# Kernel optimization log

Hardware: AMD Instinct MI355X
Metric: run time of the kernel (lower is better)

Reference implementation:

```python
import jax, jax.numpy as jnp
import numpy as np

NUM_EXPERTS = 32
TOP_K = 4
HIDDEN = 2048
INTER = 768
N_TOKENS = 2048
NORM_TOPK = True


def setup_inputs() -> dict:
    key = jax.random.key(0)
    k0, k1, k2, k3 = jax.random.split(key, 4)
    hidden_states = jax.random.normal(k0, (N_TOKENS, HIDDEN), dtype=jnp.float32)
    # router gate: Linear(hidden, num_experts), stored as (h, E)
    Wg = jax.random.normal(k1, (HIDDEN, NUM_EXPERTS), dtype=jnp.float32) * 0.02
    # per-expert merged gate_up: (E, h, 2*i); down: (E, i, h)
    Wgu = jax.random.normal(k2, (NUM_EXPERTS, HIDDEN, 2 * INTER), dtype=jnp.float32) * 0.02
    Wd = jax.random.normal(k3, (NUM_EXPERTS, INTER, HIDDEN), dtype=jnp.float32) * 0.02
    return {"hidden_states": hidden_states, "Wg": Wg, "Wgu": Wgu, "Wd": Wd}


def reference(hidden_states, Wg, Wgu, Wd):
    E = Wgu.shape[0]
    # ---- routing ----
    router_logits = hidden_states @ Wg                       # (N, E)
    probs = jax.nn.softmax(router_logits.astype(jnp.float32), axis=-1)
    topk_w, topk_idx = jax.lax.top_k(probs, TOP_K)           # (N, K)
    if NORM_TOPK:
        topk_w = topk_w / jnp.sum(topk_w, axis=-1, keepdims=True)
    topk_w = topk_w.astype(hidden_states.dtype)
    # dense combine weights: (N, E), zero where expert not selected
    combine = jnp.einsum("nke,nk->ne", jax.nn.one_hot(topk_idx, E, dtype=topk_w.dtype), topk_w)
    # ---- experts (dense dispatch, zero-weighted combine == gather/scatter math) ----
    gate_up = jnp.einsum("nh,ehf->nef", hidden_states, Wgu)  # (N, E, 2i)
    gate, up = jnp.split(gate_up, 2, axis=-1)                # (N, E, i) each
    y = jax.nn.silu(gate) * up                               # SiluAndMul
    y = y * combine[:, :, None]                              # apply routing weight before down-proj (linear -> equivalent)
    out = jnp.einsum("nef,efh->nh", y, Wd)                   # (N, h)
    return out
```

## Files before the change

kernel.cpp:

```cpp
#include <hip/hip_runtime.h>
#include <hip/hip_bf16.h>

#define NE 32
#define TOPK 4
#define HID 2048
#define INTER 768
#define NT 2048
#define MAXTILE 64

typedef float f32x4 __attribute__((ext_vector_type(4)));
typedef float f32x2 __attribute__((ext_vector_type(2)));
typedef unsigned int u32x4 __attribute__((ext_vector_type(4)));
typedef unsigned int u32x2 __attribute__((ext_vector_type(2)));
typedef short short8 __attribute__((ext_vector_type(8)));
typedef __bf16 bf16x8 __attribute__((ext_vector_type(8)));

__device__ inline unsigned short f2bf(float f) {
  unsigned u = __builtin_bit_cast(unsigned, f);
  u += 0x7fffu + ((u >> 16) & 1u);
  return (unsigned short)(u >> 16);
}
__device__ inline unsigned pack2(unsigned short a, unsigned short b) {
  return (unsigned)a | ((unsigned)b << 16);
}
__device__ inline f32x4 mfma_bf16(short8 a, short8 b, f32x4 c) {
  return __builtin_amdgcn_mfma_f32_16x16x32_bf16(
      __builtin_bit_cast(bf16x8, a), __builtin_bit_cast(bf16x8, b), c, 0, 0, 0);
}
__device__ inline void gload16(const void* g, void* l) {
  __builtin_amdgcn_global_load_lds(
      (const __attribute__((address_space(1))) void*)g,
      (__attribute__((address_space(3))) void*)l, 16, 0, 0);
}
__device__ inline bool locate(const int* __restrict__ counts, int tile, int& e,
                              int& m0, int& base, int& ne) {
  int tl = tile;
  base = 0;
  for (e = 0; e < NE; ++e) {
    const int c = counts[e];
    const int nt = (c + 255) >> 8;
    if (tl < nt) {
      m0 = tl << 8;
      ne = c;
      return true;
    }
    tl -= nt;
    base += c;
  }
  return false;
}

__global__ __launch_bounds__(64) void k_router(const float* __restrict__ X,
                                               const float* __restrict__ Wg,
                                               int* __restrict__ expert_of,
                                               float* __restrict__ weight_of,
                                               int* __restrict__ counts,
                                               unsigned short* __restrict__ Xb) {
  const int n = blockIdx.x;
  const int lane = threadIdx.x;
  const float* x = X + (size_t)n * HID;
  float acc[NE];
#pragma unroll
  for (int e = 0; e < NE; ++e) acc[e] = 0.f;
  for (int h = lane; h < HID; h += 64) {
    const float xv = x[h];
    const f32x4* wr = (const f32x4*)(Wg + (size_t)h * NE);
#pragma unroll
    for (int q = 0; q < NE / 4; ++q) {
      f32x4 w4 = wr[q];
      acc[q * 4 + 0] += xv * w4[0];
      acc[q * 4 + 1] += xv * w4[1];
      acc[q * 4 + 2] += xv * w4[2];
      acc[q * 4 + 3] += xv * w4[3];
    }
  }
  const f32x4* x4 = (const f32x4*)x;
  u32x2* xb2 = (u32x2*)(Xb + (size_t)n * HID);
#pragma unroll
  for (int it = 0; it < HID / 4 / 64; ++it) {
    const int q = it * 64 + lane;
    f32x4 v = x4[q];
    u32x2 t = {pack2(f2bf(v[0]), f2bf(v[1])), pack2(f2bf(v[2]), f2bf(v[3]))};
    xb2[q] = t;
  }
#pragma unroll
  for (int off = 32; off >= 1; off >>= 1) {
#pragma unroll
    for (int e = 0; e < NE; ++e) acc[e] += __shfl_xor(acc[e], off, 64);
  }
  if (lane == 0) {
    float m = acc[0];
#pragma unroll
    for (int e = 1; e < NE; ++e) m = fmaxf(m, acc[e]);
    unsigned used = 0;
    int idx[TOPK];
    float wv[TOPK];
    float wsum = 0.f;
    for (int k = 0; k < TOPK; ++k) {
      int best = 0;
      float bv = -1e30f;
      for (int e = 0; e < NE; ++e) {
        if (!((used >> e) & 1u) && acc[e] > bv) { bv = acc[e]; best = e; }
      }
      used |= 1u << best;
      float w = expf(bv - m);
      idx[k] = best;
      wv[k] = w;
      wsum += w;
    }
    const float inv = 1.f / wsum;
    for (int k = 0; k < TOPK; ++k) {
      expert_of[n * TOPK + k] = idx[k];
      weight_of[n * TOPK + k] = wv[k] * inv;
      atomicAdd(&counts[idx[k]], 1);
    }
  }
}

__global__ __launch_bounds__(64) void k_scatter(const int* __restrict__ expert_of,
                                                const float* __restrict__ weight_of,
                                                const int* __restrict__ counts,
                                                int* __restrict__ slot_token,
                                                float* __restrict__ slot_w) {
  const int e = blockIdx.x;
  const int lane = threadIdx.x;
  int cnt = 0;
  for (int i = 0; i < NE; ++i) cnt += (i < e) ? counts[i] : 0;
  for (int a0 = 0; a0 < NT * TOPK; a0 += 64) {
    const int a = a0 + lane;
    const bool m = (expert_of[a] == e);
    const unsigned long long bal = __ballot(m);
    if (m) {
      const int pos = cnt + __popcll(bal & ((1ull << lane) - 1ull));
      slot_token[pos] = a >> 2;
      slot_w[pos] = weight_of[a];
    }
    cnt += __popcll(bal);
  }
}

__global__ __launch_bounds__(512) void k_gemm1(const unsigned short* __restrict__ Xb,
                                               const float* __restrict__ Wgu,
                                               const int* __restrict__ slot_token,
                                               const float* __restrict__ slot_w,
                                               const int* __restrict__ counts,
                                               unsigned short* __restrict__ Y) {
  int e, m0, base, ne;
  if (!locate(counts, blockIdx.x, e, m0, base, ne)) return;
  const int n0 = blockIdx.y * 64;
  const int tid = threadIdx.x;
  const int lane = tid & 63, w = tid >> 6;
  const int wm = w >> 1, wn = w & 1;
  const int fr = lane & 15, fo = lane >> 4;
  const int lr = lane >> 3, lk = lane & 7;

  __shared__ __attribute__((aligned(16))) unsigned short As[2][256 * 64];
  __shared__ __attribute__((aligned(16))) unsigned short Bg[2][64 * 64];
  __shared__ __attribute__((aligned(16))) unsigned short Bu[2][64 * 64];

  f32x4 accg[4][2], accu[4][2];
#pragma unroll
  for (int i = 0; i < 4; ++i)
#pragma unroll
    for (int j = 0; j < 2; ++j) {
      f32x4 z = {0.f, 0.f, 0.f, 0.f};
      accg[i][j] = z;
      accu[i][j] = z;
    }

  const unsigned short* asrc[4];
#pragma unroll
  for (int i = 0; i < 4; ++i) {
    const int ra = (w * 4 + i) * 8 + lr;
    const int tok = slot_token[base + min(m0 + ra, ne - 1)];
    asrc[i] = Xb + (size_t)tok * HID + ((lk ^ (ra & 7)) << 3);
  }

  const int np = tid & 31, kg = (tid >> 5) & 7, rg = tid >> 8;
  const float* bsrc = Wgu + (size_t)e * HID * (2 * INTER) +
                      (size_t)(kg * 8) * (2 * INTER) + rg * INTER + n0 + 2 * np;
  const int n_a = 2 * np, n_b = 2 * np + 1;
  const int wofa = n_a * 64 + ((kg ^ (n_a & 7)) << 3);
  const int wofb = n_b * 64 + ((kg ^ (n_b & 7)) << 3);

  auto stage_a = [&](int t, int b) {
#pragma unroll
    for (int i = 0; i < 4; ++i) gload16(asrc[i] + t * 64, &As[b][(w * 4 + i) * 512]);
  };
  auto load_b = [&](int t, f32x2* bv) {
    const float* bp = bsrc + (size_t)(t * 64) * (2 * INTER);
#pragma unroll
    for (int j = 0; j < 8; ++j) bv[j] = *(const f32x2*)(bp + (size_t)j * (2 * INTER));
  };
  auto pack_write = [&](const f32x2* bv, int b) {
    u32x4 ta = {pack2(f2bf(bv[0][0]), f2bf(bv[1][0])), pack2(f2bf(bv[2][0]), f2bf(bv[3][0])),
                pack2(f2bf(bv[4][0]), f2bf(bv[5][0])), pack2(f2bf(bv[6][0]), f2bf(bv[7][0]))};
    u32x4 tb = {pack2(f2bf(bv[0][1]), f2bf(bv[1][1])), pack2(f2bf(bv[2][1]), f2bf(bv[3][1])),
                pack2(f2bf(bv[4][1]), f2bf(bv[5][1])), pack2(f2bf(bv[6][1]), f2bf(bv[7][1]))};
    unsigned short* Bd = rg ? Bu[b] : Bg[b];
    *(u32x4*)&Bd[wofa] = ta;
    *(u32x4*)&Bd[wofb] = tb;
  };
  auto do_mfma = [&](int b) {
#pragma unroll
    for (int ks = 0; ks < 2; ++ks) {
      const int c = ks * 4 + fo;
      short8 a[4], bg[2], bu[2];
#pragma unroll
      for (int mi = 0; mi < 4; ++mi) {
        const int row = wm * 64 + mi * 16 + fr;
        a[mi] = *(const short8*)&As[b][row * 64 + ((c ^ (row & 7)) << 3)];
      }
#pragma unroll
      for (int ni = 0; ni < 2; ++ni) {
        const int row = wn * 32 + ni * 16 + fr;
        const int off = row * 64 + ((c ^ (row & 7)) << 3);
        bg[ni] = *(const short8*)&Bg[b][off];
        bu[ni] = *(const short8*)&Bu[b][off];
      }
#pragma unroll
      for (int mi = 0; mi < 4; ++mi)
#pragma unroll
        for (int ni = 0; ni < 2; ++ni) {
          accg[mi][ni] = mfma_bf16(a[mi], bg[ni], accg[mi][ni]);
          accu[mi][ni] = mfma_bf16(a[mi], bu[ni], accu[mi][ni]);
        }
    }
  };

  const int NS = HID / 64;
  {
    f32x2 bv[8];
    stage_a(0, 0);
    load_b(0, bv);
    pack_write(bv, 0);
  }
  __syncthreads();
#pragma unroll 2
  for (int t = 0; t < NS; ++t) {
    const int cur = t & 1, nxt = cur ^ 1;
    f32x2 bv[8];
    const bool more = (t + 1 < NS);
    if (more) {
      stage_a(t + 1, nxt);
      load_b(t + 1, bv);
    }
    __builtin_amdgcn_sched_barrier(0);
    do_mfma(cur);
    if (more) pack_write(bv, nxt);
    __syncthreads();
  }

#pragma unroll
  for (int mi = 0; mi < 4; ++mi) {
#pragma unroll
    for (int j = 0; j < 4; ++j) {
      const int gm = m0 + wm * 64 + mi * 16 + fo * 4 + j;
      if (gm < ne) {
        const float wgt = slot_w[base + gm];
        unsigned short* yp = Y + (size_t)(base + gm) * INTER + n0 + wn * 32;
#pragma unroll
        for (int ni = 0; ni < 2; ++ni) {
          const float g = accg[mi][ni][j];
          const float u = accu[mi][ni][j];
          const float yv = (g / (1.0f + __expf(-g))) * u * wgt;
          yp[ni * 16 + fr] = f2bf(yv);
        }
      }
    }
  }
}

__global__ __launch_bounds__(512) void k_gemm2(const unsigned short* __restrict__ Y,
                                               const float* __restrict__ Wd,
                                               const int* __restrict__ slot_token,
                                               const int* __restrict__ counts,
                                               float* __restrict__ out) {
  int e, m0, base, ne;
  if (!locate(counts, blockIdx.x, e, m0, base, ne)) return;
  const int n0 = blockIdx.y * 128;
  const int tid = threadIdx.x;
  const int lane = tid & 63, w = tid >> 6;
  const int wm = w >> 1, wn = w & 1;
  const int fr = lane & 15, fo = lane >> 4;
  const int lr = lane >> 3, lk = lane & 7;

  __shared__ __attribute__((aligned(16))) unsigned short As[2][256 * 64];
  __shared__ __attribute__((aligned(16))) unsigned short Bs[2][128 * 64];

  f32x4 acc[4][4];
#pragma unroll
  for (int i = 0; i < 4; ++i)
#pragma unroll
    for (int j = 0; j < 4; ++j) {
      f32x4 z = {0.f, 0.f, 0.f, 0.f};
      acc[i][j] = z;
    }

  const unsigned short* asrc[4];
#pragma unroll
  for (int i = 0; i < 4; ++i) {
    const int ra = (w * 4 + i) * 8 + lr;
    const int grow = base + min(m0 + ra, ne - 1);
    asrc[i] = Y + (size_t)grow * INTER + ((lk ^ (ra & 7)) << 3);
  }

  const int np = tid & 63, kg = tid >> 6;
  const float* bsrc = Wd + (size_t)e * INTER * HID + (size_t)(kg * 8) * HID + n0 + 2 * np;
  const int n_a = 2 * np, n_b = 2 * np + 1;
  const int wofa = n_a * 64 + ((kg ^ (n_a & 7)) << 3);
  const int wofb = n_b * 64 + ((kg ^ (n_b & 7)) << 3);

  auto stage_a = [&](int t, int b) {
#pragma unroll
    for (int i = 0; i < 4; ++i) gload16(asrc[i] + t * 64, &As[b][(w * 4 + i) * 512]);
  };
  auto load_b = [&](int t, f32x2* bv) {
    const float* bp = bsrc + (size_t)(t * 64) * HID;
#pragma unroll
    for (int j = 0; j < 8; ++j) bv[j] = *(const f32x2*)(bp + (size_t)j * HID);
  };
  auto pack_write = [&](const f32x2* bv, int b) {
    u32x4 ta = {pack2(f2bf(bv[0][0]), f2bf(bv[1][0])), pack2(f2bf(bv[2][0]), f2bf(bv[3][0])),
                pack2(f2bf(bv[4][0]), f2bf(bv[5][0])), pack2(f2bf(bv[6][0]), f2bf(bv[7][0]))};
    u32x4 tb = {pack2(f2bf(bv[0][1]), f2bf(bv[1][1])), pack2(f2bf(bv[2][1]), f2bf(bv[3][1])),
                pack2(f2bf(bv[4][1]), f2bf(bv[5][1])), pack2(f2bf(bv[6][1]), f2bf(bv[7][1]))};
    *(u32x4*)&Bs[b][wofa] = ta;
    *(u32x4*)&Bs[b][wofb] = tb;
  };
  auto do_mfma = [&](int b) {
#pragma unroll
    for (int ks = 0; ks < 2; ++ks) {
      const int c = ks * 4 + fo;
      short8 a[4], bb[4];
#pragma unroll
      for (int mi = 0; mi < 4; ++mi) {
        const int row = wm * 64 + mi * 16 + fr;
        a[mi] = *(const short8*)&As[b][row * 64 + ((c ^ (row & 7)) << 3)];
      }
#pragma unroll
      for (int ni = 0; ni < 4; ++ni) {
        const int row = wn * 64 + ni * 16 + fr;
        bb[ni] = *(const short8*)&Bs[b][row * 64 + ((c ^ (row & 7)) << 3)];
      }
#pragma unroll
      for (int mi = 0; mi < 4; ++mi)
#pragma unroll
        for (int ni = 0; ni < 4; ++ni) acc[mi][ni] = mfma_bf16(a[mi], bb[ni], acc[mi][ni]);
    }
  };

  const int NS = INTER / 64;
  {
    f32x2 bv[8];
    stage_a(0, 0);
    load_b(0, bv);
    pack_write(bv, 0);
  }
  __syncthreads();
#pragma unroll 2
  for (int t = 0; t < NS; ++t) {
    const int cur = t & 1, nxt = cur ^ 1;
    f32x2 bv[8];
    const bool more = (t + 1 < NS);
    if (more) {
      stage_a(t + 1, nxt);
      load_b(t + 1, bv);
    }
    __builtin_amdgcn_sched_barrier(0);
    do_mfma(cur);
    if (more) pack_write(bv, nxt);
    __syncthreads();
  }

#pragma unroll
  for (int mi = 0; mi < 4; ++mi) {
#pragma unroll
    for (int j = 0; j < 4; ++j) {
      const int gm = m0 + wm * 64 + mi * 16 + fo * 4 + j;
      if (gm < ne) {
        const int tok = slot_token[base + gm];
        float* op = out + (size_t)tok * HID + n0 + wn * 64;
#pragma unroll
        for (int ni = 0; ni < 4; ++ni) atomicAdd(&op[ni * 16 + fr], acc[mi][ni][j]);
      }
    }
  }
}

extern "C" void kernel_launch(void* const* d_in, const int* in_sizes, int n_in,
                              void* d_out, int out_size, void* d_ws, size_t ws_size,
                              hipStream_t stream) {
  (void)in_sizes; (void)n_in; (void)ws_size;
  const float* X = (const float*)d_in[0];
  const float* Wg = (const float*)d_in[1];
  const float* Wgu = (const float*)d_in[2];
  const float* Wd = (const float*)d_in[3];
  float* out = (float*)d_out;

  char* ws = (char*)d_ws;
  int* counts = (int*)(ws + 0);
  int* expert_of = (int*)(ws + 2048);
  float* weight_of = (float*)(ws + 2048 + 32768);
  int* slot_token = (int*)(ws + 2048 + 2 * 32768);
  float* slot_w = (float*)(ws + 2048 + 3 * 32768);
  unsigned short* Xb = (unsigned short*)(ws + 133120);
  unsigned short* Yb = (unsigned short*)(ws + 8521728);

  hipMemsetAsync(counts, 0, 128, stream);
  hipMemsetAsync(d_out, 0, (size_t)out_size * sizeof(float), stream);

  k_router<<<NT, 64, 0, stream>>>(X, Wg, expert_of, weight_of, counts, Xb);
  k_scatter<<<NE, 64, 0, stream>>>(expert_of, weight_of, counts, slot_token, slot_w);
  k_gemm1<<<dim3(MAXTILE, INTER / 64), 512, 0, stream>>>(Xb, Wgu, slot_token, slot_w,
                                                         counts, Yb);
  k_gemm2<<<dim3(MAXTILE, HID / 128), 512, 0, stream>>>(Yb, Wd, slot_token, counts, out);
}
```

Before: 536.6 us.

## Halve M tile to 128 and prefetch B two stages ahead with manual waitcnt

Shrinks the per-block token tile in both expert GEMMs from 256 to 128 rows, which doubles the number of tiles per expert, shrinks the accumulators and shared memory, and adds an occupancy hint of 4 blocks. The B-weight register prefetch now runs two K-steps ahead using a double register buffer, with explicit vmcnt/lgkmcnt waits and raw barriers in place of __syncthreads, so global load latency is hidden behind the MFMAs. The cost is that each B weight tile is re-read and re-converted by twice as many blocks, there are more atomics per output, and the hand-counted waitcnt values must match the real number of outstanding loads or the results will be wrong.

```diff
diff --git a/kernel.cpp b/kernel.cpp
--- a/kernel.cpp
+++ b/kernel.cpp
@@ -6,7 +6,7 @@
 #define HID 2048
 #define INTER 768
 #define NT 2048
-#define MAXTILE 64
+#define MAXTILE 96
 
 typedef float f32x4 __attribute__((ext_vector_type(4)));
 typedef float f32x2 __attribute__((ext_vector_type(2)));
@@ -38,9 +38,9 @@
   base = 0;
   for (e = 0; e < NE; ++e) {
     const int c = counts[e];
-    const int nt = (c + 255) >> 8;
+    const int nt = (c + 127) >> 7;
     if (tl < nt) {
-      m0 = tl << 8;
+      m0 = tl << 7;
       ne = c;
       return true;
     }
@@ -139,12 +139,10 @@
   }
 }
 
-__global__ __launch_bounds__(512) void k_gemm1(const unsigned short* __restrict__ Xb,
-                                               const float* __restrict__ Wgu,
-                                               const int* __restrict__ slot_token,
-                                               const float* __restrict__ slot_w,
-                                               const int* __restrict__ counts,
-                                               unsigned short* __restrict__ Y) {
+__global__ __launch_bounds__(512, 4) void k_gemm1(
+    const unsigned short* __restrict__ Xb, const float* __restrict__ Wgu,
+    const int* __restrict__ slot_token, const float* __restrict__ slot_w,
+    const int* __restrict__ counts, unsigned short* __restrict__ Y) {
   int e, m0, base, ne;
   if (!locate(counts, blockIdx.x, e, m0, base, ne)) return;
   const int n0 = blockIdx.y * 64;
@@ -154,13 +152,13 @@
   const int fr = lane & 15, fo = lane >> 4;
   const int lr = lane >> 3, lk = lane & 7;
 
-  __shared__ __attribute__((aligned(16))) unsigned short As[2][256 * 64];
+  __shared__ __attribute__((aligned(16))) unsigned short As[2][128 * 64];
   __shared__ __attribute__((aligned(16))) unsigned short Bg[2][64 * 64];
   __shared__ __attribute__((aligned(16))) unsigned short Bu[2][64 * 64];
 
-  f32x4 accg[4][2], accu[4][2];
-#pragma unroll
-  for (int i = 0; i < 4; ++i)
+  f32x4 accg[2][2], accu[2][2];
+#pragma unroll
+  for (int i = 0; i < 2; ++i)
 #pragma unroll
     for (int j = 0; j < 2; ++j) {
       f32x4 z = {0.f, 0.f, 0.f, 0.f};
@@ -168,10 +166,10 @@
       accu[i][j] = z;
     }
 
-  const unsigned short* asrc[4];
-#pragma unroll
-  for (int i = 0; i < 4; ++i) {
-    const int ra = (w * 4 + i) * 8 + lr;
+  const unsigned short* asrc[2];
+#pragma unroll
+  for (int i = 0; i < 2; ++i) {
+    const int ra = (w * 2 + i) * 8 + lr;
     const int tok = slot_token[base + min(m0 + ra, ne - 1)];
     asrc[i] = Xb + (size_t)tok * HID + ((lk ^ (ra & 7)) << 3);
   }
@@ -185,7 +183,7 @@
 
   auto stage_a = [&](int t, int b) {
 #pragma unroll
-    for (int i = 0; i < 4; ++i) gload16(asrc[i] + t * 64, &As[b][(w * 4 + i) * 512]);
+    for (int i = 0; i < 2; ++i) gload16(asrc[i] + t * 64, &As[b][(w * 2 + i) * 512]);
   };
   auto load_b = [&](int t, f32x2* bv) {
     const float* bp = bsrc + (size_t)(t * 64) * (2 * INTER);
@@ -205,10 +203,10 @@
 #pragma unroll
     for (int ks = 0; ks < 2; ++ks) {
       const int c = ks * 4 + fo;
-      short8 a[4], bg[2], bu[2];
-#pragma unroll
-      for (int mi = 0; mi < 4; ++mi) {
-        const int row = wm * 64 + mi * 16 + fr;
+      short8 a[2], bg[2], bu[2];
+#pragma unroll
+      for (int mi = 0; mi < 2; ++mi) {
+        const int row = wm * 32 + mi * 16 + fr;
         a[mi] = *(const short8*)&As[b][row * 64 + ((c ^ (row & 7)) << 3)];
       }
 #pragma unroll
@@ -219,7 +217,7 @@
         bu[ni] = *(const short8*)&Bu[b][off];
       }
 #pragma unroll
-      for (int mi = 0; mi < 4; ++mi)
+      for (int mi = 0; mi < 2; ++mi)
 #pragma unroll
         for (int ni = 0; ni < 2; ++ni) {
           accg[mi][ni] = mfma_bf16(a[mi], bg[ni], accg[mi][ni]);
@@ -229,33 +227,40 @@
   };
 
   const int NS = HID / 64;
+  f32x2 bv[2][8];
+  stage_a(0, 0);
+  load_b(0, bv[0]);
+  load_b(1, bv[1]);
+  pack_write(bv[0], 0);
+  asm volatile("s_waitcnt lgkmcnt(0)" ::: "memory");
+  __builtin_amdgcn_s_barrier();
+
+#pragma unroll 2
+  for (int t = 0; t < NS - 2; ++t) {
+    const int cur = t & 1, nxt = cur ^ 1;
+    stage_a(t + 1, nxt);
+    load_b(t + 2, bv[cur]);
+    asm volatile("s_waitcnt vmcnt(18)" ::: "memory");
+    do_mfma(cur);
+    pack_write(bv[nxt], nxt);
+    asm volatile("s_waitcnt lgkmcnt(0)" ::: "memory");
+    __builtin_amdgcn_s_barrier();
+  }
   {
-    f32x2 bv[8];
-    stage_a(0, 0);
-    load_b(0, bv);
-    pack_write(bv, 0);
-  }
-  __syncthreads();
-#pragma unroll 2
-  for (int t = 0; t < NS; ++t) {
-    const int cur = t & 1, nxt = cur ^ 1;
-    f32x2 bv[8];
-    const bool more = (t + 1 < NS);
-    if (more) {
-      stage_a(t + 1, nxt);
-      load_b(t + 1, bv);
-    }
-    __builtin_amdgcn_sched_barrier(0);
+    const int t = NS - 2, cur = t & 1, nxt = cur ^ 1;
+    stage_a(t + 1, nxt);
+    asm volatile("s_waitcnt vmcnt(10)" ::: "memory");
     do_mfma(cur);
-    if (more) pack_write(bv, nxt);
+    pack_write(bv[nxt], nxt);
     __syncthreads();
   }
-
-#pragma unroll
-  for (int mi = 0; mi < 4; ++mi) {
+  do_mfma((NS - 1) & 1);
+
+#pragma unroll
+  for (int mi = 0; mi < 2; ++mi) {
 #pragma unroll
     for (int j = 0; j < 4; ++j) {
-      const int gm = m0 + wm * 64 + mi * 16 + fo * 4 + j;
+      const int gm = m0 + wm * 32 + mi * 16 + fo * 4 + j;
       if (gm < ne) {
         const float wgt = slot_w[base + gm];
         unsigned short* yp = Y + (size_t)(base + gm) * INTER + n0 + wn * 32;
@@ -271,11 +276,10 @@
   }
 }
 
-__global__ __launch_bounds__(512) void k_gemm2(const unsigned short* __restrict__ Y,
-                                               const float* __restrict__ Wd,
-                                               const int* __restrict__ slot_token,
-                                               const int* __restrict__ counts,
-                                               float* __restrict__ out) {
+__global__ __launch_bounds__(512, 4) void k_gemm2(
+    const unsigned short* __restrict__ Y, const float* __restrict__ Wd,
+    const int* __restrict__ slot_token, const int* __restrict__ counts,
+    float* __restrict__ out) {
   int e, m0, base, ne;
   if (!locate(counts, blockIdx.x, e, m0, base, ne)) return;
   const int n0 = blockIdx.y * 128;
@@ -285,22 +289,22 @@
   const int fr = lane & 15, fo = lane >> 4;
   const int lr = lane >> 3, lk = lane & 7;
 
-  __shared__ __attribute__((aligned(16))) unsigned short As[2][256 * 64];
+  __shared__ __attribute__((aligned(16))) unsigned short As[2][128 * 64];
   __shared__ __attribute__((aligned(16))) unsigned short Bs[2][128 * 64];
 
-  f32x4 acc[4][4];
-#pragma unroll
-  for (int i = 0; i < 4; ++i)
+  f32x4 acc[2][4];
+#pragma unroll
+  for (int i = 0; i < 2; ++i)
 #pragma unroll
     for (int j = 0; j < 4; ++j) {
       f32x4 z = {0.f, 0.f, 0.f, 0.f};
       acc[i][j] = z;
     }
 
-  const unsigned short* asrc[4];
-#pragma unroll
-  for (int i = 0; i < 4; ++i) {
-    const int ra = (w * 4 + i) * 8 + lr;
+  const unsigned short* asrc[2];
+#pragma unroll
+  for (int i = 0; i < 2; ++i) {
+    const int ra = (w * 2 + i) * 8 + lr;
     const int grow = base + min(m0 + ra, ne - 1);
     asrc[i] = Y + (size_t)grow * INTER + ((lk ^ (ra & 7)) << 3);
   }
@@ -313,7 +317,7 @@
 
   auto stage_a = [&](int t, int b) {
 #pragma unroll
-    for (int i = 0; i < 4; ++i) gload16(asrc[i] + t * 64, &As[b][(w * 4 + i) * 512]);
+    for (int i = 0; i < 2; ++i) gload16(asrc[i] + t * 64, &As[b][(w * 2 + i) * 512]);
   };
   auto load_b = [&](int t, f32x2* bv) {
     const float* bp = bsrc + (size_t)(t * 64) * HID;
@@ -332,10 +336,10 @@
 #pragma unroll
     for (int ks = 0; ks < 2; ++ks) {
       const int c = ks * 4 + fo;
-      short8 a[4], bb[4];
-#pragma unroll
-      for (int mi = 0; mi < 4; ++mi) {
-        const int row = wm * 64 + mi * 16 + fr;
+      short8 a[2], bb[4];
+#pragma unroll
+      for (int mi = 0; mi < 2; ++mi) {
+        const int row = wm * 32 + mi * 16 + fr;
         a[mi] = *(const short8*)&As[b][row * 64 + ((c ^ (row & 7)) << 3)];
       }
 #pragma unroll
@@ -344,40 +348,47 @@
         bb[ni] = *(const short8*)&Bs[b][row * 64 + ((c ^ (row & 7)) << 3)];
       }
 #pragma unroll
-      for (int mi = 0; mi < 4; ++mi)
+      for (int mi = 0; mi < 2; ++mi)
 #pragma unroll
         for (int ni = 0; ni < 4; ++ni) acc[mi][ni] = mfma_bf16(a[mi], bb[ni], acc[mi][ni]);
     }
   };
 
   const int NS = INTER / 64;
+  f32x2 bv[2][8];
+  stage_a(0, 0);
+  load_b(0, bv[0]);
+  load_b(1, bv[1]);
+  pack_write(bv[0], 0);
+  asm volatile("s_waitcnt lgkmcnt(0)" ::: "memory");
+  __builtin_amdgcn_s_barrier();
+
+#pragma unroll 2
+  for (int t = 0; t < NS - 2; ++t) {
+    const int cur = t & 1, nxt = cur ^ 1;
+    stage_a(t + 1, nxt);
+    load_b(t + 2, bv[cur]);
+    asm volatile("s_waitcnt vmcnt(18)" ::: "memory");
+    do_mfma(cur);
+    pack_write(bv[nxt], nxt);
+    asm volatile("s_waitcnt lgkmcnt(0)" ::: "memory");
+    __builtin_amdgcn_s_barrier();
+  }
   {
-    f32x2 bv[8];
-    stage_a(0, 0);
-    load_b(0, bv);
-    pack_write(bv, 0);
-  }
-  __syncthreads();
-#pragma unroll 2
-  for (int t = 0; t < NS; ++t) {
-    const int cur = t & 1, nxt = cur ^ 1;
-    f32x2 bv[8];
-    const bool more = (t + 1 < NS);
-    if (more) {
-      stage_a(t + 1, nxt);
-      load_b(t + 1, bv);
-    }
-    __builtin_amdgcn_sched_barrier(0);
+    const int t = NS - 2, cur = t & 1, nxt = cur ^ 1;
+    stage_a(t + 1, nxt);
+    asm volatile("s_waitcnt vmcnt(10)" ::: "memory");
     do_mfma(cur);
-    if (more) pack_write(bv, nxt);
+    pack_write(bv[nxt], nxt);
     __syncthreads();
   }
-
-#pragma unroll
-  for (int mi = 0; mi < 4; ++mi) {
+  do_mfma((NS - 1) & 1);
+
+#pragma unroll
+  for (int mi = 0; mi < 2; ++mi) {
 #pragma unroll
     for (int j = 0; j < 4; ++j) {
-      const int gm = m0 + wm * 64 + mi * 16 + fo * 4 + j;
+      const int gm = m0 + wm * 32 + mi * 16 + fo * 4 + j;
       if (gm < ne) {
         const int tok = slot_token[base + gm];
         float* op = out + (size_t)tok * HID + n0 + wn * 64;
```

New measurement: 508.2 us. 1.06x faster.

## Single-buffer A tile, two-stage B register prefetch, setprio around MFMAs, fuse output zeroing

Applied to the files above, without the earlier changes.

Both grouped GEMM kernels drop the double-buffered A tile in LDS and use a single buffer. The main loop is rebuilt around explicit s_waitcnt/s_barrier points, with B prefetched two steps ahead in registers, s_setprio raised around the MFMA block, and launch bounds of 4 blocks per CU. The output memset is folded into the router kernel, which saves a separate memset launch. The aim is lower LDS use for higher occupancy and better overlap of global loads with MFMA. The cost is an extra barrier per iteration and fragile hand-written vmcnt counts.

```diff
diff --git a/kernel.cpp b/kernel.cpp
--- a/kernel.cpp
+++ b/kernel.cpp
@@ -55,10 +55,16 @@
                                                int* __restrict__ expert_of,
                                                float* __restrict__ weight_of,
                                                int* __restrict__ counts,
-                                               unsigned short* __restrict__ Xb) {
+                                               unsigned short* __restrict__ Xb,
+                                               float* __restrict__ out) {
   const int n = blockIdx.x;
   const int lane = threadIdx.x;
   const float* x = X + (size_t)n * HID;
+  f32x4* orow = (f32x4*)(out + (size_t)n * HID);
+  const f32x4 z4 = {0.f, 0.f, 0.f, 0.f};
+#pragma unroll
+  for (int i = 0; i < HID / 4 / 64; ++i) orow[i * 64 + lane] = z4;
+
   float acc[NE];
 #pragma unroll
   for (int e = 0; e < NE; ++e) acc[e] = 0.f;
@@ -139,12 +145,10 @@
   }
 }
 
-__global__ __launch_bounds__(512) void k_gemm1(const unsigned short* __restrict__ Xb,
-                                               const float* __restrict__ Wgu,
-                                               const int* __restrict__ slot_token,
-                                               const float* __restrict__ slot_w,
-                                               const int* __restrict__ counts,
-                                               unsigned short* __restrict__ Y) {
+__global__ __launch_bounds__(512, 4) void k_gemm1(
+    const unsigned short* __restrict__ Xb, const float* __restrict__ Wgu,
+    const int* __restrict__ slot_token, const float* __restrict__ slot_w,
+    const int* __restrict__ counts, unsigned short* __restrict__ Y) {
   int e, m0, base, ne;
   if (!locate(counts, blockIdx.x, e, m0, base, ne)) return;
   const int n0 = blockIdx.y * 64;
@@ -154,9 +158,8 @@
   const int fr = lane & 15, fo = lane >> 4;
   const int lr = lane >> 3, lk = lane & 7;
 
-  __shared__ __attribute__((aligned(16))) unsigned short As[2][256 * 64];
-  __shared__ __attribute__((aligned(16))) unsigned short Bg[2][64 * 64];
-  __shared__ __attribute__((aligned(16))) unsigned short Bu[2][64 * 64];
+  __shared__ __attribute__((aligned(16))) unsigned short As[256 * 64];
+  __shared__ __attribute__((aligned(16))) unsigned short Bs[2][128 * 64];
 
   f32x4 accg[4][2], accu[4][2];
 #pragma unroll
@@ -179,13 +182,13 @@
   const int np = tid & 31, kg = (tid >> 5) & 7, rg = tid >> 8;
   const float* bsrc = Wgu + (size_t)e * HID * (2 * INTER) +
                       (size_t)(kg * 8) * (2 * INTER) + rg * INTER + n0 + 2 * np;
-  const int n_a = 2 * np, n_b = 2 * np + 1;
-  const int wofa = n_a * 64 + ((kg ^ (n_a & 7)) << 3);
-  const int wofb = n_b * 64 + ((kg ^ (n_b & 7)) << 3);
-
-  auto stage_a = [&](int t, int b) {
-#pragma unroll
-    for (int i = 0; i < 4; ++i) gload16(asrc[i] + t * 64, &As[b][(w * 4 + i) * 512]);
+  const int rowa = rg * 64 + 2 * np, rowb = rowa + 1;
+  const int wofa = rowa * 64 + ((kg ^ (rowa & 7)) << 3);
+  const int wofb = rowb * 64 + ((kg ^ (rowb & 7)) << 3);
+
+  auto stage_a = [&](int t) {
+#pragma unroll
+    for (int i = 0; i < 4; ++i) gload16(asrc[i] + t * 64, &As[(w * 4 + i) * 512]);
   };
   auto load_b = [&](int t, f32x2* bv) {
     const float* bp = bsrc + (size_t)(t * 64) * (2 * INTER);
@@ -197,9 +200,8 @@
                 pack2(f2bf(bv[4][0]), f2bf(bv[5][0])), pack2(f2bf(bv[6][0]), f2bf(bv[7][0]))};
     u32x4 tb = {pack2(f2bf(bv[0][1]), f2bf(bv[1][1])), pack2(f2bf(bv[2][1]), f2bf(bv[3][1])),
                 pack2(f2bf(bv[4][1]), f2bf(bv[5][1])), pack2(f2bf(bv[6][1]), f2bf(bv[7][1]))};
-    unsigned short* Bd = rg ? Bu[b] : Bg[b];
-    *(u32x4*)&Bd[wofa] = ta;
-    *(u32x4*)&Bd[wofb] = tb;
+    *(u32x4*)&Bs[b][wofa] = ta;
+    *(u32x4*)&Bs[b][wofb] = tb;
   };
   auto do_mfma = [&](int b) {
 #pragma unroll
@@ -209,15 +211,16 @@
 #pragma unroll
       for (int mi = 0; mi < 4; ++mi) {
         const int row = wm * 64 + mi * 16 + fr;
-        a[mi] = *(const short8*)&As[b][row * 64 + ((c ^ (row & 7)) << 3)];
+        a[mi] = *(const short8*)&As[row * 64 + ((c ^ (row & 7)) << 3)];
       }
 #pragma unroll
       for (int ni = 0; ni < 2; ++ni) {
         const int row = wn * 32 + ni * 16 + fr;
         const int off = row * 64 + ((c ^ (row & 7)) << 3);
-        bg[ni] = *(const short8*)&Bg[b][off];
-        bu[ni] = *(const short8*)&Bu[b][off];
-      }
+        bg[ni] = *(const short8*)&Bs[b][off];
+        bu[ni] = *(const short8*)&Bs[b][off + 64 * 64];
+      }
+      __builtin_amdgcn_s_setprio(1);
 #pragma unroll
       for (int mi = 0; mi < 4; ++mi)
 #pragma unroll
@@ -225,31 +228,43 @@
           accg[mi][ni] = mfma_bf16(a[mi], bg[ni], accg[mi][ni]);
           accu[mi][ni] = mfma_bf16(a[mi], bu[ni], accu[mi][ni]);
         }
+      __builtin_amdgcn_s_setprio(0);
     }
   };
 
   const int NS = HID / 64;
+  f32x2 bv[8];
+  load_b(0, bv);
+  stage_a(0);
+  pack_write(bv, 0);
+  load_b(1, bv);
+  asm volatile("s_waitcnt vmcnt(8)" ::: "memory");
+  asm volatile("s_waitcnt lgkmcnt(0)" ::: "memory");
+  __builtin_amdgcn_s_barrier();
+
+#pragma unroll 2
+  for (int t = 0; t < NS - 2; ++t) {
+    const int cur = t & 1;
+    do_mfma(cur);
+    pack_write(bv, cur ^ 1);
+    asm volatile("s_waitcnt lgkmcnt(0)" ::: "memory");
+    __builtin_amdgcn_s_barrier();
+    stage_a(t + 1);
+    load_b(t + 2, bv);
+    asm volatile("s_waitcnt vmcnt(8)" ::: "memory");
+    __builtin_amdgcn_s_barrier();
+  }
   {
-    f32x2 bv[8];
-    stage_a(0, 0);
-    load_b(0, bv);
-    pack_write(bv, 0);
-  }
-  __syncthreads();
-#pragma unroll 2
-  for (int t = 0; t < NS; ++t) {
-    const int cur = t & 1, nxt = cur ^ 1;
-    f32x2 bv[8];
-    const bool more = (t + 1 < NS);
-    if (more) {
-      stage_a(t + 1, nxt);
-      load_b(t + 1, bv);
-    }
-    __builtin_amdgcn_sched_barrier(0);
+    const int cur = (NS - 2) & 1;
     do_mfma(cur);
-    if (more) pack_write(bv, nxt);
-    __syncthreads();
-  }
+    pack_write(bv, cur ^ 1);
+    asm volatile("s_waitcnt lgkmcnt(0)" ::: "memory");
+    __builtin_amdgcn_s_barrier();
+    stage_a(NS - 1);
+    asm volatile("s_waitcnt vmcnt(0)" ::: "memory");
+    __builtin_amdgcn_s_barrier();
+  }
+  do_mfma((NS - 1) & 1);
 
 #pragma unroll
   for (int mi = 0; mi < 4; ++mi) {
@@ -271,11 +286,10 @@
   }
 }
 
-__global__ __launch_bounds__(512) void k_gemm2(const unsigned short* __restrict__ Y,
-                                               const float* __restrict__ Wd,
-                                               const int* __restrict__ slot_token,
-                                               const int* __restrict__ counts,
-                                               float* __restrict__ out) {
+__global__ __launch_bounds__(512, 4) void k_gemm2(
+    const unsigned short* __restrict__ Y, const float* __restrict__ Wd,
+    const int* __restrict__ slot_token, const int* __restrict__ counts,
+    float* __restrict__ out) {
   int e, m0, base, ne;
   if (!locate(counts, blockIdx.x, e, m0, base, ne)) return;
   const int n0 = blockIdx.y * 128;
@@ -285,7 +299,7 @@
   const int fr = lane & 15, fo = lane >> 4;
   const int lr = lane >> 3, lk = lane & 7;
 
-  __shared__ __attribute__((aligned(16))) unsigned short As[2][256 * 64];
+  __shared__ __attribute__((aligned(16))) unsigned short As[256 * 64];
   __shared__ __attribute__((aligned(16))) unsigned short Bs[2][128 * 64];
 
   f32x4 acc[4][4];
@@ -305,15 +319,15 @@
     asrc[i] = Y + (size_t)grow * INTER + ((lk ^ (ra & 7)) << 3);
   }
 
-  const int np = tid & 63, kg = tid >> 6;
+  const int np = tid & 63, kg = (tid >> 6) & 7;
   const float* bsrc = Wd + (size_t)e * INTER * HID + (size_t)(kg * 8) * HID + n0 + 2 * np;
-  const int n_a = 2 * np, n_b = 2 * np + 1;
-  const int wofa = n_a * 64 + ((kg ^ (n_a & 7)) << 3);
-  const int wofb = n_b * 64 + ((kg ^ (n_b & 7)) << 3);
-
-  auto stage_a = [&](int t, int b) {
-#pragma unroll
-    for (int i = 0; i < 4; ++i) gload16(asrc[i] + t * 64, &As[b][(w * 4 + i) * 512]);
+  const int rowa = 2 * np, rowb = rowa + 1;
+  const int wofa = rowa * 64 + ((kg ^ (rowa & 7)) << 3);
+  const int wofb = rowb * 64 + ((kg ^ (rowb & 7)) << 3);
+
+  auto stage_a = [&](int t) {
+#pragma unroll
+    for (int i = 0; i < 4; ++i) gload16(asrc[i] + t * 64, &As[(w * 4 + i) * 512]);
   };
   auto load_b = [&](int t, f32x2* bv) {
     const float* bp = bsrc + (size_t)(t * 64) * HID;
@@ -336,42 +350,55 @@
 #pragma unroll
       for (int mi = 0; mi < 4; ++mi) {
         const int row = wm * 64 + mi * 16 + fr;
-        a[mi] = *(const short8*)&As[b][row * 64 + ((c ^ (row & 7)) << 3)];
+        a[mi] = *(const short8*)&As[row * 64 + ((c ^ (row & 7)) << 3)];
       }
 #pragma unroll
       for (int ni = 0; ni < 4; ++ni) {
         const int row = wn * 64 + ni * 16 + fr;
         bb[ni] = *(const short8*)&Bs[b][row * 64 + ((c ^ (row & 7)) << 3)];
       }
+      __builtin_amdgcn_s_setprio(1);
 #pragma unroll
       for (int mi = 0; mi < 4; ++mi)
 #pragma unroll
         for (int ni = 0; ni < 4; ++ni) acc[mi][ni] = mfma_bf16(a[mi], bb[ni], acc[mi][ni]);
+      __builtin_amdgcn_s_setprio(0);
     }
   };
 
   const int NS = INTER / 64;
+  f32x2 bv[8];
+  load_b(0, bv);
+  stage_a(0);
+  pack_write(bv, 0);
+  load_b(1, bv);
+  asm volatile("s_waitcnt vmcnt(8)" ::: "memory");
+  asm volatile("s_waitcnt lgkmcnt(0)" ::: "memory");
+  __builtin_amdgcn_s_barrier();
+
+#pragma unroll 2
+  for (int t = 0; t < NS - 2; ++t) {
+    const int cur = t & 1;
+    do_mfma(cur);
+    pack_write(bv, cur ^ 1);
+    asm volatile("s_waitcnt lgkmcnt(0)" ::: "memory");
+    __builtin_amdgcn_s_barrier();
+    stage_a(t + 1);
+    load_b(t + 2, bv);
+    asm volatile("s_waitcnt vmcnt(8)" ::: "memory");
+    __builtin_amdgcn_s_barrier();
+  }
   {
-    f32x2 bv[8];
-    stage_a(0, 0);
-    load_b(0, bv);
-    pack_write(bv, 0);
-  }
-  __syncthreads();
-#pragma unroll 2
-  for (int t = 0; t < NS; ++t) {
-    const int cur = t & 1, nxt = cur ^ 1;
-    f32x2 bv[8];
-    const bool more = (t + 1 < NS);
-    if (more) {
-      stage_a(t + 1, nxt);
-      load_b(t + 1, bv);
-    }
-    __builtin_amdgcn_sched_barrier(0);
+    const int cur = (NS - 2) & 1;
     do_mfma(cur);
-    if (more) pack_write(bv, nxt);
-    __syncthreads();
-  }
+    pack_write(bv, cur ^ 1);
+    asm volatile("s_waitcnt lgkmcnt(0)" ::: "memory");
+    __builtin_amdgcn_s_barrier();
+    stage_a(NS - 1);
+    asm volatile("s_waitcnt vmcnt(0)" ::: "memory");
+    __builtin_amdgcn_s_barrier();
+  }
+  do_mfma((NS - 1) & 1);
 
 #pragma unroll
   for (int mi = 0; mi < 4; ++mi) {
@@ -391,7 +418,7 @@
 extern "C" void kernel_launch(void* const* d_in, const int* in_sizes, int n_in,
                               void* d_out, int out_size, void* d_ws, size_t ws_size,
                               hipStream_t stream) {
-  (void)in_sizes; (void)n_in; (void)ws_size;
+  (void)in_sizes; (void)n_in; (void)ws_size; (void)out_size;
   const float* X = (const float*)d_in[0];
   const float* Wg = (const float*)d_in[1];
   const float* Wgu = (const float*)d_in[2];
@@ -408,9 +435,8 @@
   unsigned short* Yb = (unsigned short*)(ws + 8521728);
 
   hipMemsetAsync(counts, 0, 128, stream);
-  hipMemsetAsync(d_out, 0, (size_t)out_size * sizeof(float), stream);
-
-  k_router<<<NT, 64, 0, stream>>>(X, Wg, expert_of, weight_of, counts, Xb);
+
+  k_router<<<NT, 64, 0, stream>>>(X, Wg, expert_of, weight_of, counts, Xb, out);
   k_scatter<<<NE, 64, 0, stream>>>(expert_of, weight_of, counts, slot_token, slot_w);
   k_gemm1<<<dim3(MAXTILE, INTER / 64), 512, 0, stream>>>(Xb, Wgu, slot_token, slot_w,
                                                          counts, Yb);
```

Result: slower. 1.119 ms (+108.5%).
